# Performance work log

Hardware: AMD Instinct MI355X
Metric: run time of the kernel (lower is better)

Reference implementation:

```python
import jax, jax.numpy as jnp
import numpy as np

CUTOFF = 4.0
RBF_N = 32          # distance_embedding_size == D_rbf
F_DIM = 128         # hidden_size
N_ATOMS = 20000
N_PROBES = 100000
N_EDGES = 262144
LN_EPS = 1e-5


def setup_inputs() -> dict:
    key = jax.random.key(0)
    ks = jax.random.split(key, 20)
    s = 0.02
    inp = {
        "diff_pi": jax.random.normal(ks[0], (N_EDGES, 3), jnp.float32),
        "S_JK": jax.random.normal(ks[1], (N_ATOMS, F_DIM), jnp.float32),
        "V_JK": jax.random.normal(ks[2], (N_ATOMS, 3, F_DIM), jnp.float32),
        "atom_idx": jax.random.randint(ks[3], (N_EDGES,), 0, N_ATOMS),
        "probe_idx": jax.random.randint(ks[4], (N_EDGES,), 0, N_PROBES),
        "num_probes": N_PROBES,
        # state branch params
        "w_s1": jax.random.normal(ks[5], (3 * F_DIM, F_DIM), jnp.float32) * s,
        "b_s1": jnp.zeros((F_DIM,), jnp.float32),
        "g_ln": jnp.ones((F_DIM,), jnp.float32),
        "b_ln": jnp.zeros((F_DIM,), jnp.float32),
        "w_s2": jax.random.normal(ks[6], (F_DIM, F_DIM), jnp.float32) * s,
        "b_s2": jnp.zeros((F_DIM,), jnp.float32),
        # filter branch params
        "w_f1": jax.random.normal(ks[7], (RBF_N, F_DIM), jnp.float32) * s,
        "b_f1": jnp.zeros((F_DIM,), jnp.float32),
        "w_f2": jax.random.normal(ks[8], (F_DIM, F_DIM), jnp.float32) * s,
        "b_f2": jnp.zeros((F_DIM,), jnp.float32),
        # output head params
        "w_o1": jax.random.normal(ks[9], (F_DIM, F_DIM // 2), jnp.float32) * s,
        "b_o1": jnp.zeros((F_DIM // 2,), jnp.float32),
        "w_o2": jax.random.normal(ks[10], (F_DIM // 2, 1), jnp.float32) * s,
        "b_o2": jnp.zeros((1,), jnp.float32),
        "final_bias": jnp.array([-6.1], jnp.float32),
    }
    return inp


def reference(diff_pi, S_JK, V_JK, atom_idx, probe_idx, num_probes,
              w_s1, b_s1, g_ln, b_ln, w_s2, b_s2,
              w_f1, b_f1, w_f2, b_f2,
              w_o1, b_o1, w_o2, b_o2, final_bias):
    silu = jax.nn.silu
    # edge distances
    sq = (diff_pi ** 2).sum(-1)                       # [E]
    dist = jnp.sqrt(sq)                               # [E] exact distance
    dist_safe = jnp.sqrt(sq + 1e-8)[:, None]          # [E,1]
    r_hat = diff_pi / dist_safe                       # [E,3]

    # sinc RBF expansion: sin(n*pi*d/cutoff)/d, n=1..RBF_N
    n = jnp.arange(1, RBF_N + 1, dtype=diff_pi.dtype) # [D]
    e_pi = jnp.sin(dist[:, None] * n * (jnp.pi / CUTOFF)) / dist[:, None]  # [E,D]

    # gather atom features to edges
    n_i = jnp.sqrt((V_JK ** 2).sum(1) + 1e-8)         # [N,F]
    n_e = n_i[atom_idx]                               # [E,F]
    V_e = V_JK[atom_idx]                              # [E,3,F]
    q_pi = (V_e * r_hat[:, :, None]).sum(1)           # [E,F]
    S_e = S_JK[atom_idx]                              # [E,F]

    # state branch: Linear -> LayerNorm -> SiLU -> Linear
    h = jnp.concatenate([S_e, n_e, q_pi], axis=-1)    # [E,3F]
    u = h @ w_s1 + b_s1                               # [E,F]
    mu = u.mean(-1, keepdims=True)
    var = ((u - mu) ** 2).mean(-1, keepdims=True)
    u_norm = (u - mu) / jnp.sqrt(var + LN_EPS) * g_ln + b_ln
    state = silu(u_norm) @ w_s2 + b_s2                # [E,F]

    # filter branch (no normalization -> absolute distance scale)
    W = silu(e_pi @ w_f1 + b_f1) @ w_f2 + b_f2        # [E,F]

    # fuse + output head
    m = (silu((W * state) @ w_o1 + b_o1) @ w_o2 + b_o2)[:, 0]  # [E]

    x = dist / CUTOFF
    env = 1.0 - 21.0 * x ** 5 + 35.0 * x ** 6 - 15.0 * x ** 7
    env = jnp.where(dist < CUTOFF, env, jnp.zeros_like(env))
    m_w = m * env

    # scatter-add to probes
    rho = jax.ops.segment_sum(m_w, probe_idx, num_segments=num_probes)
    return rho + final_bias[0]
```

## Files before the change

### kernel.cpp

```cpp
#include <hip/hip_runtime.h>

#define EPB     64
#define E_TOTAL 262144
#define NPROBE  100000
#define N_ATOMS 20000

#define ASTR   136
#define A2_O   0
#define F1_O   8704
#define EPI_O  17408
#define LDS_SH 19968

#define WS1_O  0
#define WS2_O  49152
#define WF1_O  65536
#define WF2_O  69632
#define WO1_O  86016
#define WT_TOT 94208
#define PQ_O   WT_TOT

typedef __attribute__((ext_vector_type(8))) short          short8;
typedef __attribute__((ext_vector_type(8))) unsigned short ushort8;
typedef __attribute__((ext_vector_type(4))) float          floatx4;

#define MFMA16(a, b, c) __builtin_amdgcn_mfma_f32_16x16x32_bf16((a), (b), (c), 0, 0, 0)

__device__ __forceinline__ short f2bf(float x) {
    unsigned u = __builtin_bit_cast(unsigned, x);
    u = (u + 0x7FFFu + ((u >> 16) & 1u)) >> 16;
    return (short)(unsigned short)u;
}
__device__ __forceinline__ unsigned pk2(float lo, float hi) {
    return __builtin_amdgcn_perm(__builtin_bit_cast(unsigned, hi),
                                 __builtin_bit_cast(unsigned, lo), 0x07060302u);
}
__device__ __forceinline__ float bf2f(unsigned short u) {
    return __builtin_bit_cast(float, ((unsigned)u) << 16);
}
__device__ __forceinline__ float silu_f(float x) { return x / (1.0f + __expf(-x)); }

struct F8 { float v[8]; };
__device__ __forceinline__ F8 ld8(const float* __restrict__ p) {
    F8 r;
    const float4 a = *(const float4*)p;
    const float4 b = *(const float4*)(p + 4);
    r.v[0] = a.x; r.v[1] = a.y; r.v[2] = a.z; r.v[3] = a.w;
    r.v[4] = b.x; r.v[5] = b.y; r.v[6] = b.z; r.v[7] = b.w;
    return r;
}

__global__ void cfr_prep_w(const float* __restrict__ w_s1, const float* __restrict__ w_s2,
                           const float* __restrict__ w_f1, const float* __restrict__ w_f2,
                           const float* __restrict__ w_o1,
                           const float* __restrict__ fb, float* __restrict__ out,
                           unsigned short* __restrict__ wt) {
    int i = blockIdx.x * 256 + threadIdx.x;
    if (i < NPROBE) out[i] = fb[0];
    if (i < WT_TOT) {
        float v;
        if (i < WS2_O)      { int n = i / 384, k = i - n * 384;          v = w_s1[k * 128 + n]; }
        else if (i < WF1_O) { int j = i - WS2_O, n = j >> 7, k = j & 127; v = w_s2[k * 128 + n]; }
        else if (i < WF2_O) { int j = i - WF1_O, n = j >> 5, k = j & 31;  v = w_f1[k * 128 + n]; }
        else if (i < WO1_O) { int j = i - WF2_O, n = j >> 7, k = j & 127; v = w_f2[k * 128 + n]; }
        else                { int j = i - WO1_O, n = j >> 7, k = j & 127; v = w_o1[k * 64 + n]; }
        wt[i] = (unsigned short)f2bf(v);
    }
}

__global__ __launch_bounds__(256, 1) void cfr_prep_pq(
    const float* __restrict__ S, const float* __restrict__ V,
    const float* __restrict__ b_s1,
    const unsigned short* __restrict__ wt, unsigned short* __restrict__ pq)
{
    __shared__ __align__(16) unsigned short bufH[64 * 264];
    __shared__ __align__(16) unsigned short bufV[192 * 136];

    const int t    = threadIdx.x;
    const int a0   = blockIdx.x * 64;
    const int wave = t >> 6;
    const int lane = t & 63;
    const int q    = lane >> 4;
    const int c16  = lane & 15;

#pragma unroll
    for (int it = 0; it < 4; ++it) {
        int idx = it * 256 + t;
        int al = idx >> 4, f8 = (idx & 15) * 8;
        int a = a0 + al;
        ushort8 sS, sN, s0, s1, s2;
        if (a < N_ATOMS) {
            F8 s  = ld8(S + a * 128 + f8);
            F8 v0 = ld8(V + a * 384 + f8);
            F8 v1 = ld8(V + a * 384 + 128 + f8);
            F8 v2 = ld8(V + a * 384 + 256 + f8);
#pragma unroll
            for (int j = 0; j < 8; ++j) {
                sS[j] = (unsigned short)f2bf(s.v[j]);
                sN[j] = (unsigned short)f2bf(sqrtf(v0.v[j]*v0.v[j] + v1.v[j]*v1.v[j] + v2.v[j]*v2.v[j] + 1e-8f));
                s0[j] = (unsigned short)f2bf(v0.v[j]);
                s1[j] = (unsigned short)f2bf(v1.v[j]);
                s2[j] = (unsigned short)f2bf(v2.v[j]);
            }
        } else {
#pragma unroll
            for (int j = 0; j < 8; ++j) { sS[j]=0; sN[j]=0; s0[j]=0; s1[j]=0; s2[j]=0; }
        }
        *(ushort8*)&bufH[al * 264 + f8]        = sS;
        *(ushort8*)&bufH[al * 264 + 128 + f8]  = sN;
        *(ushort8*)&bufV[(al) * 136 + f8]       = s0;
        *(ushort8*)&bufV[(64 + al) * 136 + f8]  = s1;
        *(ushort8*)&bufV[(128 + al) * 136 + f8] = s2;
    }
    __syncthreads();

    const floatx4 zero4 = {0.f, 0.f, 0.f, 0.f};
    float bs1c[2];
#pragma unroll
    for (int ni = 0; ni < 2; ++ni) bs1c[ni] = b_s1[wave * 32 + ni * 16 + c16];

    {
        floatx4 pacc[4][2];
#pragma unroll
        for (int mi = 0; mi < 4; ++mi) { pacc[mi][0] = zero4; pacc[mi][1] = zero4; }
#pragma unroll
        for (int kk = 0; kk < 8; ++kk) {
            short8 bfr[2], af[4];
#pragma unroll
            for (int ni = 0; ni < 2; ++ni) {
                int n = wave * 32 + ni * 16 + c16;
                bfr[ni] = *(const short8*)&wt[WS1_O + n * 384 + kk * 32 + q * 8];
            }
#pragma unroll
            for (int mi = 0; mi < 4; ++mi)
                af[mi] = *(const short8*)&bufH[(mi * 16 + c16) * 264 + kk * 32 + q * 8];
#pragma unroll
            for (int mi = 0; mi < 4; ++mi)
#pragma unroll
                for (int ni = 0; ni < 2; ++ni)
                    pacc[mi][ni] = MFMA16(af[mi], bfr[ni], pacc[mi][ni]);
        }
#pragma unroll
        for (int mi = 0; mi < 4; ++mi)
#pragma unroll
            for (int r = 0; r < 4; ++r) {
                int a = a0 + mi * 16 + q * 4 + r;
                if (a < N_ATOMS)
#pragma unroll
                    for (int ni = 0; ni < 2; ++ni) {
                        int col = wave * 32 + ni * 16 + c16;
                        pq[a * 512 + col] = (unsigned short)f2bf(pacc[mi][ni][r] + bs1c[ni]);
                    }
            }
    }

    short8 bq[4][2];
#pragma unroll
    for (int kk = 0; kk < 4; ++kk)
#pragma unroll
        for (int ni = 0; ni < 2; ++ni) {
            int n = wave * 32 + ni * 16 + c16;
            bq[kk][ni] = *(const short8*)&wt[WS1_O + n * 384 + 256 + kk * 32 + q * 8];
        }
#pragma unroll
    for (int d = 0; d < 3; ++d) {
        floatx4 qacc[4][2];
#pragma unroll
        for (int mi = 0; mi < 4; ++mi) { qacc[mi][0] = zero4; qacc[mi][1] = zero4; }
#pragma unroll
        for (int kk = 0; kk < 4; ++kk) {
            short8 af[4];
#pragma unroll
            for (int mi = 0; mi < 4; ++mi)
                af[mi] = *(const short8*)&bufV[(d * 64 + mi * 16 + c16) * 136 + kk * 32 + q * 8];
#pragma unroll
            for (int mi = 0; mi < 4; ++mi)
#pragma unroll
                for (int ni = 0; ni < 2; ++ni)
                    qacc[mi][ni] = MFMA16(af[mi], bq[kk][ni], qacc[mi][ni]);
        }
#pragma unroll
        for (int mi = 0; mi < 4; ++mi)
#pragma unroll
            for (int r = 0; r < 4; ++r) {
                int a = a0 + mi * 16 + q * 4 + r;
                if (a < N_ATOMS)
#pragma unroll
                    for (int ni = 0; ni < 2; ++ni) {
                        int col = wave * 32 + ni * 16 + c16;
                        pq[a * 512 + (1 + d) * 128 + col] = (unsigned short)f2bf(qacc[mi][ni][r]);
                    }
            }
    }
}

__global__ __launch_bounds__(256, 4) void cfr_main(
    const float* __restrict__ diff,
    const int* __restrict__ atom_idx, const int* __restrict__ probe_idx,
    const unsigned short* __restrict__ wt, const unsigned short* __restrict__ pq,
    const float* __restrict__ g_ln, const float* __restrict__ b_ln,
    const float* __restrict__ b_s2, const float* __restrict__ b_f1,
    const float* __restrict__ b_f2, const float* __restrict__ b_o1,
    const float* __restrict__ w_o2, const float* __restrict__ b_o2,
    float* __restrict__ out)
{
    __shared__ __align__(16) unsigned short LDSu[LDS_SH];
    float* mpart = (float*)&LDSu[EPI_O];

    const int t    = threadIdx.x;
    const int e0   = blockIdx.x * EPB;
    const int wave = t >> 6;
    const int lane = t & 63;
    const int q    = lane >> 4;
    const int c16  = lane & 15;
    const floatx4 zero4 = {0.f, 0.f, 0.f, 0.f};

    {
        const int el = t >> 2;
        const int c0 = (t & 3) * 32;
        const int eg = e0 + el;
        const int a  = atom_idx[eg];
        float dx = diff[eg * 3 + 0], dy = diff[eg * 3 + 1], dz = diff[eg * 3 + 2];
        float sq   = dx * dx + dy * dy + dz * dz;
        float dist = sqrtf(sq);
        float rinv = rsqrtf(sq + 1e-8f);
        float rx = dx * rinv, ry = dy * rinv, rz = dz * rinv;

        const ushort8* pqr = (const ushort8*)(pq + a * 512 + c0);
        float u[32];
#pragma unroll
        for (int g = 0; g < 4; ++g) {
            ushort8 v = pqr[g];
#pragma unroll
            for (int j = 0; j < 8; ++j) u[g * 8 + j] = bf2f(v[j]);
        }
#pragma unroll
        for (int g = 0; g < 4; ++g) {
            ushort8 v = pqr[16 + g];
#pragma unroll
            for (int j = 0; j < 8; ++j) u[g * 8 + j] = fmaf(bf2f(v[j]), rx, u[g * 8 + j]);
        }
#pragma unroll
        for (int g = 0; g < 4; ++g) {
            ushort8 v = pqr[32 + g];
#pragma unroll
            for (int j = 0; j < 8; ++j) u[g * 8 + j] = fmaf(bf2f(v[j]), ry, u[g * 8 + j]);
        }
#pragma unroll
        for (int g = 0; g < 4; ++g) {
            ushort8 v = pqr[48 + g];
#pragma unroll
            for (int j = 0; j < 8; ++j) u[g * 8 + j] = fmaf(bf2f(v[j]), rz, u[g * 8 + j]);
        }
        float s = 0.f, s2 = 0.f;
#pragma unroll
        for (int j = 0; j < 32; ++j) { s += u[j]; s2 = fmaf(u[j], u[j], s2); }
        s  += __shfl_xor(s, 1);  s  += __shfl_xor(s, 2);
        s2 += __shfl_xor(s2, 1); s2 += __shfl_xor(s2, 2);
        float mu = s * (1.f / 128.f);
        float rstd = rsqrtf(s2 * (1.f / 128.f) - mu * mu + 1e-5f);
        const float4* gp = (const float4*)(g_ln + c0);
        const float4* bp = (const float4*)(b_ln + c0);
        unsigned pko[16];
#pragma unroll
        for (int g4 = 0; g4 < 8; ++g4) {
            float4 gg = gp[g4], bb = bp[g4];
            float y0 = silu_f((u[g4 * 4 + 0] - mu) * rstd * gg.x + bb.x);
            float y1 = silu_f((u[g4 * 4 + 1] - mu) * rstd * gg.y + bb.y);
            float y2 = silu_f((u[g4 * 4 + 2] - mu) * rstd * gg.z + bb.z);
            float y3 = silu_f((u[g4 * 4 + 3] - mu) * rstd * gg.w + bb.w);
            pko[g4 * 2 + 0] = pk2(y0, y1);
            pko[g4 * 2 + 1] = pk2(y2, y3);
        }
        uint4* dst = (uint4*)&LDSu[A2_O + el * ASTR + c0];
        dst[0] = make_uint4(pko[0], pko[1], pko[2], pko[3]);
        dst[1] = make_uint4(pko[4], pko[5], pko[6], pko[7]);
        dst[2] = make_uint4(pko[8], pko[9], pko[10], pko[11]);
        dst[3] = make_uint4(pko[12], pko[13], pko[14], pko[15]);
        float inv = 1.0f / dist;
        float sv[8];
#pragma unroll
        for (int j = 0; j < 8; ++j) {
            float nf = (float)((t & 3) * 8 + j + 1);
            sv[j] = __sinf(dist * nf * 0.785398163397448f) * inv;
        }
        *(uint4*)&LDSu[EPI_O + el * 40 + (t & 3) * 8] =
            make_uint4(pk2(sv[0], sv[1]), pk2(sv[2], sv[3]), pk2(sv[4], sv[5]), pk2(sv[6], sv[7]));
    }
    __syncthreads();

    {
        short8 ae[4], be[2];
#pragma unroll
        for (int mi = 0; mi < 4; ++mi)
            ae[mi] = *(const short8*)&LDSu[EPI_O + (mi * 16 + c16) * 40 + q * 8];
#pragma unroll
        for (int ni = 0; ni < 2; ++ni) {
            int n = wave * 32 + ni * 16 + c16;
            be[ni] = *(const short8*)&wt[WF1_O + n * 32 + q * 8];
        }
        floatx4 facc[4][2];
#pragma unroll
        for (int mi = 0; mi < 4; ++mi)
#pragma unroll
            for (int ni = 0; ni < 2; ++ni)
                facc[mi][ni] = MFMA16(ae[mi], be[ni], zero4);
        float bf1c[2];
#pragma unroll
        for (int ni = 0; ni < 2; ++ni) bf1c[ni] = b_f1[wave * 32 + ni * 16 + c16];
#pragma unroll
        for (int mi = 0; mi < 4; ++mi)
#pragma unroll
            for (int r = 0; r < 4; ++r) {
                int row = mi * 16 + q * 4 + r;
#pragma unroll
                for (int ni = 0; ni < 2; ++ni) {
                    float v = facc[mi][ni][r] + bf1c[ni];
                    LDSu[F1_O + row * ASTR + (wave * 32 + ni * 16 + c16)] =
                        (unsigned short)(__builtin_bit_cast(unsigned, silu_f(v)) >> 16);
                }
            }
    }
    __syncthreads();

    {
        floatx4 sacc[4][2], wacc[4][2];
#pragma unroll
        for (int mi = 0; mi < 4; ++mi)
#pragma unroll
            for (int ni = 0; ni < 2; ++ni) { sacc[mi][ni] = zero4; wacc[mi][ni] = zero4; }
#pragma unroll
        for (int kk = 0; kk < 4; ++kk) {
            short8 a2f[4], f1f[4], b2[2], bw[2];
#pragma unroll
            for (int ni = 0; ni < 2; ++ni) {
                int n = wave * 32 + ni * 16 + c16;
                b2[ni] = *(const short8*)&wt[WS2_O + n * 128 + kk * 32 + q * 8];
                bw[ni] = *(const short8*)&wt[WF2_O + n * 128 + kk * 32 + q * 8];
            }
#pragma unroll
            for (int mi = 0; mi < 4; ++mi) {
                a2f[mi] = *(const short8*)&LDSu[A2_O + (mi * 16 + c16) * ASTR + kk * 32 + q * 8];
                f1f[mi] = *(const short8*)&LDSu[F1_O + (mi * 16 + c16) * ASTR + kk * 32 + q * 8];
            }
#pragma unroll
            for (int mi = 0; mi < 4; ++mi)
#pragma unroll
                for (int ni = 0; ni < 2; ++ni) {
                    sacc[mi][ni] = MFMA16(a2f[mi], b2[ni], sacc[mi][ni]);
                    wacc[mi][ni] = MFMA16(f1f[mi], bw[ni], wacc[mi][ni]);
                }
        }
        __syncthreads();
        float bs2c[2], bf2c[2];
#pragma unroll
        for (int ni = 0; ni < 2; ++ni) {
            int col = wave * 32 + ni * 16 + c16;
            bs2c[ni] = b_s2[col]; bf2c[ni] = b_f2[col];
        }
#pragma unroll
        for (int mi = 0; mi < 4; ++mi)
#pragma unroll
            for (int r = 0; r < 4; ++r) {
                int row = mi * 16 + q * 4 + r;
#pragma unroll
                for (int ni = 0; ni < 2; ++ni) {
                    float g = (sacc[mi][ni][r] + bs2c[ni]) * (wacc[mi][ni][r] + bf2c[ni]);
                    LDSu[A2_O + row * ASTR + (wave * 32 + ni * 16 + c16)] =
                        (unsigned short)(__builtin_bit_cast(unsigned, g) >> 16);
                }
            }
    }
    __syncthreads();

    {
        const int n2 = wave * 16 + c16;
        floatx4 oacc[4];
#pragma unroll
        for (int mi = 0; mi < 4; ++mi) oacc[mi] = zero4;
#pragma unroll
        for (int kk = 0; kk < 4; ++kk) {
            short8 bfr = *(const short8*)&wt[WO1_O + n2 * 128 + kk * 32 + q * 8];
#pragma unroll
            for (int mi = 0; mi < 4; ++mi) {
                short8 af = *(const short8*)&LDSu[A2_O + (mi * 16 + c16) * ASTR + kk * 32 + q * 8];
                oacc[mi] = MFMA16(af, bfr, oacc[mi]);
            }
        }
        float bo1c = b_o1[n2], wo2c = w_o2[n2];
#pragma unroll
        for (int mi = 0; mi < 4; ++mi)
#pragma unroll
            for (int r = 0; r < 4; ++r) {
                float s = silu_f(oacc[mi][r] + bo1c) * wo2c;
#pragma unroll
                for (int d = 1; d < 16; d <<= 1) s += __shfl_xor(s, d, 64);
                if (c16 == 0) mpart[(mi * 16 + q * 4 + r) * 4 + wave] = s;
            }
    }
    __syncthreads();

    if (t < EPB) {
        int eg = e0 + t;
        float m = mpart[t * 4 + 0] + mpart[t * 4 + 1] + mpart[t * 4 + 2] + mpart[t * 4 + 3] + b_o2[0];
        float dx = diff[eg * 3 + 0], dy = diff[eg * 3 + 1], dz = diff[eg * 3 + 2];
        float dist = sqrtf(dx * dx + dy * dy + dz * dz);
        float x  = dist * 0.25f;
        float x2 = x * x, x4 = x2 * x2;
        float x5 = x4 * x, x6 = x5 * x, x7 = x6 * x;
        float env = 1.0f - 21.0f * x5 + 35.0f * x6 - 15.0f * x7;
        env = (dist < 4.0f) ? env : 0.0f;
        float mw = m * env;
        if (mw != 0.f) unsafeAtomicAdd(&out[probe_idx[eg]], mw);
    }
}

extern "C" void kernel_launch(void* const* d_in, const int* in_sizes, int n_in,
                              void* d_out, int out_size, void* d_ws, size_t ws_size,
                              hipStream_t stream) {
    const float* diff    = (const float*)d_in[0];
    const float* S_JK    = (const float*)d_in[1];
    const float* V_JK    = (const float*)d_in[2];
    const int*   atom_i  = (const int*)d_in[3];
    const int*   probe_i = (const int*)d_in[4];
    const float* w_s1 = (const float*)d_in[6];
    const float* b_s1 = (const float*)d_in[7];
    const float* g_ln = (const float*)d_in[8];
    const float* b_ln = (const float*)d_in[9];
    const float* w_s2 = (const float*)d_in[10];
    const float* b_s2 = (const float*)d_in[11];
    const float* w_f1 = (const float*)d_in[12];
    const float* b_f1 = (const float*)d_in[13];
    const float* w_f2 = (const float*)d_in[14];
    const float* b_f2 = (const float*)d_in[15];
    const float* w_o1 = (const float*)d_in[16];
    const float* b_o1 = (const float*)d_in[17];
    const float* w_o2 = (const float*)d_in[18];
    const float* b_o2 = (const float*)d_in[19];
    const float* fbias = (const float*)d_in[20];
    float* out = (float*)d_out;

    unsigned short* wt = (unsigned short*)d_ws;
    unsigned short* pqp = wt + PQ_O;

    cfr_prep_w<<<(NPROBE + 255) / 256, 256, 0, stream>>>(w_s1, w_s2, w_f1, w_f2, w_o1,
                                                         fbias, out, wt);
    cfr_prep_pq<<<(N_ATOMS + 63) / 64, 256, 0, stream>>>(S_JK, V_JK, b_s1, wt, pqp);
    cfr_main<<<E_TOTAL / EPB, 256, 0, stream>>>(diff, atom_i, probe_i, wt, pqp,
        g_ln, b_ln, b_s2, b_f1, b_f2, b_o1, w_o2, b_o2, out);
}
```

Before: 242.3 us.

## Swizzle LDS tiles, shrink shared memory, pack FMA math, raise occupancy

```diff
diff --git a/kernel.cpp b/kernel.cpp
--- a/kernel.cpp
+++ b/kernel.cpp
@@ -5,11 +5,9 @@
 #define NPROBE  100000
 #define N_ATOMS 20000
 
-#define ASTR   136
 #define A2_O   0
-#define F1_O   8704
-#define EPI_O  17408
-#define LDS_SH 19968
+#define F1_O   8192
+#define LDS_SH 16384
 
 #define WS1_O  0
 #define WS2_O  49152
@@ -22,6 +20,7 @@
 typedef __attribute__((ext_vector_type(8))) short          short8;
 typedef __attribute__((ext_vector_type(8))) unsigned short ushort8;
 typedef __attribute__((ext_vector_type(4))) float          floatx4;
+typedef __attribute__((ext_vector_type(2))) float          floatx2;
 
 #define MFMA16(a, b, c) __builtin_amdgcn_mfma_f32_16x16x32_bf16((a), (b), (c), 0, 0, 0)
 
@@ -34,10 +33,18 @@
     return __builtin_amdgcn_perm(__builtin_bit_cast(unsigned, hi),
                                  __builtin_bit_cast(unsigned, lo), 0x07060302u);
 }
-__device__ __forceinline__ float bf2f(unsigned short u) {
-    return __builtin_bit_cast(float, ((unsigned)u) << 16);
-}
-__device__ __forceinline__ float silu_f(float x) { return x / (1.0f + __expf(-x)); }
+__device__ __forceinline__ floatx2 bfpair(unsigned w) {
+    floatx2 r;
+    r.x = __builtin_bit_cast(float, w << 16);
+    r.y = __builtin_bit_cast(float, w & 0xffff0000u);
+    return r;
+}
+__device__ __forceinline__ floatx2 fma2(floatx2 a, floatx2 b, floatx2 c) {
+    return __builtin_elementwise_fma(a, b, c);
+}
+__device__ __forceinline__ float silu_f(float x) {
+    return x * __builtin_amdgcn_rcpf(1.0f + __expf(-x));
+}
 
 struct F8 { float v[8]; };
 __device__ __forceinline__ F8 ld8(const float* __restrict__ p) {
@@ -67,13 +74,13 @@
     }
 }
 
-__global__ __launch_bounds__(256, 1) void cfr_prep_pq(
+__global__ __launch_bounds__(256, 2) void cfr_prep_pq(
     const float* __restrict__ S, const float* __restrict__ V,
     const float* __restrict__ b_s1,
     const unsigned short* __restrict__ wt, unsigned short* __restrict__ pq)
 {
-    __shared__ __align__(16) unsigned short bufH[64 * 264];
-    __shared__ __align__(16) unsigned short bufV[192 * 136];
+    __shared__ __align__(16) unsigned short bufH[64 * 256];
+    __shared__ __align__(16) unsigned short bufV[192 * 128];
 
     const int t    = threadIdx.x;
     const int a0   = blockIdx.x * 64;
@@ -105,15 +112,19 @@
 #pragma unroll
             for (int j = 0; j < 8; ++j) { sS[j]=0; sN[j]=0; s0[j]=0; s1[j]=0; s2[j]=0; }
         }
-        *(ushort8*)&bufH[al * 264 + f8]        = sS;
-        *(ushort8*)&bufH[al * 264 + 128 + f8]  = sN;
-        *(ushort8*)&bufV[(al) * 136 + f8]       = s0;
-        *(ushort8*)&bufV[(64 + al) * 136 + f8]  = s1;
-        *(ushort8*)&bufV[(128 + al) * 136 + f8] = s2;
+        const unsigned swH = (unsigned)((al & 7) << 4);
+        char* hrow  = (char*)bufH + al * 512;
+        char* vbase = (char*)bufV;
+        *(ushort8*)(hrow + ((f8 * 2) ^ swH))         = sS;
+        *(ushort8*)(hrow + ((256 + f8 * 2) ^ swH))   = sN;
+        *(ushort8*)(vbase + al * 256         + ((f8 * 2) ^ swH)) = s0;
+        *(ushort8*)(vbase + (64 + al) * 256  + ((f8 * 2) ^ swH)) = s1;
+        *(ushort8*)(vbase + (128 + al) * 256 + ((f8 * 2) ^ swH)) = s2;
     }
     __syncthreads();
 
     const floatx4 zero4 = {0.f, 0.f, 0.f, 0.f};
+    const unsigned swr = (unsigned)((c16 & 7) << 4);
     float bs1c[2];
 #pragma unroll
     for (int ni = 0; ni < 2; ++ni) bs1c[ni] = b_s1[wave * 32 + ni * 16 + c16];
@@ -131,8 +142,10 @@
                 bfr[ni] = *(const short8*)&wt[WS1_O + n * 384 + kk * 32 + q * 8];
             }
 #pragma unroll
-            for (int mi = 0; mi < 4; ++mi)
-                af[mi] = *(const short8*)&bufH[(mi * 16 + c16) * 264 + kk * 32 + q * 8];
+            for (int mi = 0; mi < 4; ++mi) {
+                int row = mi * 16 + c16;
+                af[mi] = *(const short8*)((const char*)bufH + row * 512 + ((unsigned)(kk * 64 + q * 16) ^ swr));
+            }
 #pragma unroll
             for (int mi = 0; mi < 4; ++mi)
 #pragma unroll
@@ -170,8 +183,10 @@
         for (int kk = 0; kk < 4; ++kk) {
             short8 af[4];
 #pragma unroll
-            for (int mi = 0; mi < 4; ++mi)
-                af[mi] = *(const short8*)&bufV[(d * 64 + mi * 16 + c16) * 136 + kk * 32 + q * 8];
+            for (int mi = 0; mi < 4; ++mi) {
+                int row = d * 64 + mi * 16 + c16;
+                af[mi] = *(const short8*)((const char*)bufV + row * 256 + ((unsigned)(kk * 64 + q * 16) ^ swr));
+            }
 #pragma unroll
             for (int mi = 0; mi < 4; ++mi)
 #pragma unroll
@@ -193,7 +208,7 @@
     }
 }
 
-__global__ __launch_bounds__(256, 4) void cfr_main(
+__global__ __launch_bounds__(256, 5) void cfr_main(
     const float* __restrict__ diff,
     const int* __restrict__ atom_idx, const int* __restrict__ probe_idx,
     const unsigned short* __restrict__ wt, const unsigned short* __restrict__ pq,
@@ -204,7 +219,6 @@
     float* __restrict__ out)
 {
     __shared__ __align__(16) unsigned short LDSu[LDS_SH];
-    float* mpart = (float*)&LDSu[EPI_O];
 
     const int t    = threadIdx.x;
     const int e0   = blockIdx.x * EPB;
@@ -216,7 +230,7 @@
 
     {
         const int el = t >> 2;
-        const int c0 = (t & 3) * 32;
+        const int cc = t & 3;
         const int eg = e0 + el;
         const int a  = atom_idx[eg];
         float dx = diff[eg * 3 + 0], dy = diff[eg * 3 + 1], dz = diff[eg * 3 + 2];
@@ -224,67 +238,78 @@
         float dist = sqrtf(sq);
         float rinv = rsqrtf(sq + 1e-8f);
         float rx = dx * rinv, ry = dy * rinv, rz = dz * rinv;
-
-        const ushort8* pqr = (const ushort8*)(pq + a * 512 + c0);
-        float u[32];
+        float rv[3] = {rx, ry, rz};
+
+        const uint4* pqr = (const uint4*)(pq + (size_t)a * 512) + cc * 4;
+        floatx2 u2[16];
 #pragma unroll
         for (int g = 0; g < 4; ++g) {
-            ushort8 v = pqr[g];
-#pragma unroll
-            for (int j = 0; j < 8; ++j) u[g * 8 + j] = bf2f(v[j]);
-        }
-#pragma unroll
-        for (int g = 0; g < 4; ++g) {
-            ushort8 v = pqr[16 + g];
-#pragma unroll
-            for (int j = 0; j < 8; ++j) u[g * 8 + j] = fmaf(bf2f(v[j]), rx, u[g * 8 + j]);
-        }
-#pragma unroll
-        for (int g = 0; g < 4; ++g) {
-            ushort8 v = pqr[32 + g];
-#pragma unroll
-            for (int j = 0; j < 8; ++j) u[g * 8 + j] = fmaf(bf2f(v[j]), ry, u[g * 8 + j]);
-        }
-#pragma unroll
-        for (int g = 0; g < 4; ++g) {
-            ushort8 v = pqr[48 + g];
-#pragma unroll
-            for (int j = 0; j < 8; ++j) u[g * 8 + j] = fmaf(bf2f(v[j]), rz, u[g * 8 + j]);
-        }
-        float s = 0.f, s2 = 0.f;
-#pragma unroll
-        for (int j = 0; j < 32; ++j) { s += u[j]; s2 = fmaf(u[j], u[j], s2); }
+            uint4 w = pqr[g];
+            u2[g * 4 + 0] = bfpair(w.x);
+            u2[g * 4 + 1] = bfpair(w.y);
+            u2[g * 4 + 2] = bfpair(w.z);
+            u2[g * 4 + 3] = bfpair(w.w);
+        }
+#pragma unroll
+        for (int d = 0; d < 3; ++d) {
+            floatx2 rr2; rr2.x = rv[d]; rr2.y = rv[d];
+#pragma unroll
+            for (int g = 0; g < 4; ++g) {
+                uint4 w = pqr[16 * (d + 1) + g];
+                u2[g * 4 + 0] = fma2(bfpair(w.x), rr2, u2[g * 4 + 0]);
+                u2[g * 4 + 1] = fma2(bfpair(w.y), rr2, u2[g * 4 + 1]);
+                u2[g * 4 + 2] = fma2(bfpair(w.z), rr2, u2[g * 4 + 2]);
+                u2[g * 4 + 3] = fma2(bfpair(w.w), rr2, u2[g * 4 + 3]);
+            }
+        }
+        floatx2 sv2 = {0.f, 0.f}, qv2 = {0.f, 0.f};
+#pragma unroll
+        for (int p = 0; p < 16; ++p) {
+            sv2 += u2[p];
+            qv2 = fma2(u2[p], u2[p], qv2);
+        }
+        float s  = sv2.x + sv2.y;
+        float s2 = qv2.x + qv2.y;
         s  += __shfl_xor(s, 1);  s  += __shfl_xor(s, 2);
         s2 += __shfl_xor(s2, 1); s2 += __shfl_xor(s2, 2);
         float mu = s * (1.f / 128.f);
         float rstd = rsqrtf(s2 * (1.f / 128.f) - mu * mu + 1e-5f);
+        floatx2 rstd2; rstd2.x = rstd; rstd2.y = rstd;
+        float nmr = -mu * rstd;
+        floatx2 nm2; nm2.x = nmr; nm2.y = nmr;
+        const int c0 = cc * 32;
         const float4* gp = (const float4*)(g_ln + c0);
         const float4* bp = (const float4*)(b_ln + c0);
         unsigned pko[16];
 #pragma unroll
         for (int g4 = 0; g4 < 8; ++g4) {
             float4 gg = gp[g4], bb = bp[g4];
-            float y0 = silu_f((u[g4 * 4 + 0] - mu) * rstd * gg.x + bb.x);
-            float y1 = silu_f((u[g4 * 4 + 1] - mu) * rstd * gg.y + bb.y);
-            float y2 = silu_f((u[g4 * 4 + 2] - mu) * rstd * gg.z + bb.z);
-            float y3 = silu_f((u[g4 * 4 + 3] - mu) * rstd * gg.w + bb.w);
-            pko[g4 * 2 + 0] = pk2(y0, y1);
-            pko[g4 * 2 + 1] = pk2(y2, y3);
-        }
-        uint4* dst = (uint4*)&LDSu[A2_O + el * ASTR + c0];
-        dst[0] = make_uint4(pko[0], pko[1], pko[2], pko[3]);
-        dst[1] = make_uint4(pko[4], pko[5], pko[6], pko[7]);
-        dst[2] = make_uint4(pko[8], pko[9], pko[10], pko[11]);
-        dst[3] = make_uint4(pko[12], pko[13], pko[14], pko[15]);
-        float inv = 1.0f / dist;
-        float sv[8];
-#pragma unroll
-        for (int j = 0; j < 8; ++j) {
-            float nf = (float)((t & 3) * 8 + j + 1);
-            sv[j] = __sinf(dist * nf * 0.785398163397448f) * inv;
-        }
-        *(uint4*)&LDSu[EPI_O + el * 40 + (t & 3) * 8] =
-            make_uint4(pk2(sv[0], sv[1]), pk2(sv[2], sv[3]), pk2(sv[4], sv[5]), pk2(sv[6], sv[7]));
+            floatx2 g0; g0.x = gg.x; g0.y = gg.y;
+            floatx2 g1; g1.x = gg.z; g1.y = gg.w;
+            floatx2 b0; b0.x = bb.x; b0.y = bb.y;
+            floatx2 b1; b1.x = bb.z; b1.y = bb.w;
+            floatx2 t0 = fma2(u2[g4 * 2 + 0], rstd2, nm2);
+            floatx2 t1 = fma2(u2[g4 * 2 + 1], rstd2, nm2);
+            floatx2 y0 = fma2(t0, g0, b0);
+            floatx2 y1 = fma2(t1, g1, b1);
+            pko[g4 * 2 + 0] = pk2(silu_f(y0.x), silu_f(y0.y));
+            pko[g4 * 2 + 1] = pk2(silu_f(y1.x), silu_f(y1.y));
+        }
+        const unsigned sw = (unsigned)((el & 7) << 4);
+        char* a2b = (char*)LDSu + el * 256;
+        *(uint4*)(a2b + (((unsigned)(cc * 64) +  0u) ^ sw)) = make_uint4(pko[0],  pko[1],  pko[2],  pko[3]);
+        *(uint4*)(a2b + (((unsigned)(cc * 64) + 16u) ^ sw)) = make_uint4(pko[4],  pko[5],  pko[6],  pko[7]);
+        *(uint4*)(a2b + (((unsigned)(cc * 64) + 32u) ^ sw)) = make_uint4(pko[8],  pko[9],  pko[10], pko[11]);
+        *(uint4*)(a2b + (((unsigned)(cc * 64) + 48u) ^ sw)) = make_uint4(pko[12], pko[13], pko[14], pko[15]);
+        float inv = __builtin_amdgcn_rcpf(dist);
+        float d8  = dist * 0.125f;
+        float nb  = (float)(cc * 8 + 1);
+        float svv[8];
+#pragma unroll
+        for (int j = 0; j < 8; ++j)
+            svv[j] = __builtin_amdgcn_sinf(d8 * (nb + (float)j)) * inv;
+        *(uint4*)((char*)LDSu + F1_O * 2 + el * 80 + cc * 16) =
+            make_uint4(pk2(svv[0], svv[1]), pk2(svv[2], svv[3]), pk2(svv[4], svv[5]), pk2(svv[6], svv[7]));
     }
     __syncthreads();
 
@@ -292,12 +317,13 @@
         short8 ae[4], be[2];
 #pragma unroll
         for (int mi = 0; mi < 4; ++mi)
-            ae[mi] = *(const short8*)&LDSu[EPI_O + (mi * 16 + c16) * 40 + q * 8];
+            ae[mi] = *(const short8*)((const char*)LDSu + F1_O * 2 + (mi * 16 + c16) * 80 + q * 16);
 #pragma unroll
         for (int ni = 0; ni < 2; ++ni) {
             int n = wave * 32 + ni * 16 + c16;
             be[ni] = *(const short8*)&wt[WF1_O + n * 32 + q * 8];
         }
+        __syncthreads();
         floatx4 facc[4][2];
 #pragma unroll
         for (int mi = 0; mi < 4; ++mi)
@@ -314,8 +340,9 @@
                 int row = mi * 16 + q * 4 + r;
 #pragma unroll
                 for (int ni = 0; ni < 2; ++ni) {
+                    int col = wave * 32 + ni * 16 + c16;
                     float v = facc[mi][ni][r] + bf1c[ni];
-                    LDSu[F1_O + row * ASTR + (wave * 32 + ni * 16 + c16)] =
+                    LDSu[F1_O + row * 128 + (col ^ ((row & 7) << 3))] =
                         (unsigned short)(__builtin_bit_cast(unsigned, silu_f(v)) >> 16);
                 }
             }
@@ -328,6 +355,7 @@
         for (int mi = 0; mi < 4; ++mi)
 #pragma unroll
             for (int ni = 0; ni < 2; ++ni) { sacc[mi][ni] = zero4; wacc[mi][ni] = zero4; }
+        const int swr = (c16 & 7) << 3;
 #pragma unroll
         for (int kk = 0; kk < 4; ++kk) {
             short8 a2f[4], f1f[4], b2[2], bw[2];
@@ -339,8 +367,10 @@
             }
 #pragma unroll
             for (int mi = 0; mi < 4; ++mi) {
-                a2f[mi] = *(const short8*)&LDSu[A2_O + (mi * 16 + c16) * ASTR + kk * 32 + q * 8];
-                f1f[mi] = *(const short8*)&LDSu[F1_O + (mi * 16 + c16) * ASTR + kk * 32 + q * 8];
+                int rr = mi * 16 + c16;
+                int colsh = (kk * 32 + q * 8) ^ swr;
+                a2f[mi] = *(const short8*)&LDSu[A2_O + rr * 128 + colsh];
+                f1f[mi] = *(const short8*)&LDSu[F1_O + rr * 128 + colsh];
             }
 #pragma unroll
             for (int mi = 0; mi < 4; ++mi)
@@ -364,8 +394,9 @@
                 int row = mi * 16 + q * 4 + r;
 #pragma unroll
                 for (int ni = 0; ni < 2; ++ni) {
+                    int col = wave * 32 + ni * 16 + c16;
                     float g = (sacc[mi][ni][r] + bs2c[ni]) * (wacc[mi][ni][r] + bf2c[ni]);
-                    LDSu[A2_O + row * ASTR + (wave * 32 + ni * 16 + c16)] =
+                    LDSu[A2_O + row * 128 + (col ^ ((row & 7) << 3))] =
                         (unsigned short)(__builtin_bit_cast(unsigned, g) >> 16);
                 }
             }
@@ -374,6 +405,7 @@
 
     {
         const int n2 = wave * 16 + c16;
+        const int swr = (c16 & 7) << 3;
         floatx4 oacc[4];
 #pragma unroll
         for (int mi = 0; mi < 4; ++mi) oacc[mi] = zero4;
@@ -382,11 +414,13 @@
             short8 bfr = *(const short8*)&wt[WO1_O + n2 * 128 + kk * 32 + q * 8];
 #pragma unroll
             for (int mi = 0; mi < 4; ++mi) {
-                short8 af = *(const short8*)&LDSu[A2_O + (mi * 16 + c16) * ASTR + kk * 32 + q * 8];
+                int rr = mi * 16 + c16;
+                short8 af = *(const short8*)&LDSu[A2_O + rr * 128 + ((kk * 32 + q * 8) ^ swr)];
                 oacc[mi] = MFMA16(af, bfr, oacc[mi]);
             }
         }
         float bo1c = b_o1[n2], wo2c = w_o2[n2];
+        float* mpart = (float*)&LDSu[F1_O];
 #pragma unroll
         for (int mi = 0; mi < 4; ++mi)
 #pragma unroll
@@ -401,7 +435,9 @@
 
     if (t < EPB) {
         int eg = e0 + t;
-        float m = mpart[t * 4 + 0] + mpart[t * 4 + 1] + mpart[t * 4 + 2] + mpart[t * 4 + 3] + b_o2[0];
+        const float* mpart = (const float*)&LDSu[F1_O];
+        float4 mp = *(const float4*)&mpart[t * 4];
+        float m = mp.x + mp.y + mp.z + mp.w + b_o2[0];
         float dx = diff[eg * 3 + 0], dy = diff[eg * 3 + 1], dz = diff[eg * 3 + 2];
         float dist = sqrtf(dx * dx + dy * dy + dz * dz);
         float x  = dist * 0.25f;
```

Result: slower. 331.8 us (+36.9%).
